# Kernel optimization log

Measured on AMD Instinct MI355X. Metric: run time of the kernel, lower is better.

Reference implementation:

```python
import jax, jax.numpy as jnp
import numpy as np

POOL = 7  # fixed 7x7 output grid, hard-coded in the original layer


def _bin_bounds(step, rlen):
    # Replicates the original bin-corner logic + empty-bin adjustment.
    i = jnp.arange(POOL, dtype=jnp.int32)
    s = i * step
    e = jnp.where(i < POOL - 1, (i + 1) * step, rlen)
    empty = s == e
    # original: grow end by 1 if room, else shrink start by 1
    e = jnp.where(empty & (e < rlen), e + 1, e)
    s = jnp.where(empty & ~(e > (i * step)) , s, s)  # no-op placeholder for clarity
    s = jnp.where(empty & ((i * step) == e), (i * step) - 1, jnp.where(empty, i * step, s))
    # simpler equivalent: if still empty after trying to grow end, shrink start
    s0 = i * step
    e0 = jnp.where(i < POOL - 1, (i + 1) * step, rlen)
    grow = empty & (e0 < rlen)
    e = jnp.where(grow, e0 + 1, e0)
    s = jnp.where(empty & ~grow, s0 - 1, s0)
    return s, e


def _pool_one(roi, fm):
    # fm: [H, W, C]; roi: [4] normalized (y1, x1, y2, x2)
    H, W, C = fm.shape
    h0 = (H * roi[0]).astype(jnp.int32)  # tf.cast to int32 truncates (floor for >=0)
    w0 = (W * roi[1]).astype(jnp.int32)
    h1 = (H * roi[2]).astype(jnp.int32)
    w1 = (W * roi[3]).astype(jnp.int32)
    rh = h1 - h0
    rw = w1 - w0
    hstep = rh // POOL
    wstep = rw // POOL
    sh, eh = _bin_bounds(hstep, rh)  # [7], region-relative
    sw, ew = _bin_bounds(wstep, rw)
    hidx = jnp.arange(H, dtype=jnp.int32)
    widx = jnp.arange(W, dtype=jnp.int32)
    rmask = (hidx[None, :] >= (h0 + sh)[:, None]) & (hidx[None, :] < (h0 + eh)[:, None])  # [7,H]
    cmask = (widx[None, :] >= (w0 + sw)[:, None]) & (widx[None, :] < (w0 + ew)[:, None])  # [7,W]
    neg = jnp.asarray(-jnp.inf, fm.dtype)
    # max over rows for each of the 7 row-bins: [7, W, C]
    t = jnp.max(jnp.where(rmask[:, :, None, None], fm[None, :, :, :], neg), axis=1)
    # max over cols for each of the 7 col-bins: [7, 7, C]
    out = jnp.max(jnp.where(cmask[None, :, :, None], t[:, None, :, :], neg), axis=2)
    return out


def setup_inputs() -> dict:
    key = jax.random.key(0)
    k_f, k_y, k_x, k_h, k_w = jax.random.split(key, 5)
    H, W, C, N = 50, 50, 1024, 300
    features = jax.random.normal(k_f, (1, H, W, C), dtype=jnp.float32)
    # well-formed normalized ROIs: y1 < y2, x1 < x2, extent in [0.2, 0.55]
    y1 = jax.random.uniform(k_y, (N,), minval=0.0, maxval=0.45)
    x1 = jax.random.uniform(k_x, (N,), minval=0.0, maxval=0.45)
    hh = jax.random.uniform(k_h, (N,), minval=0.2, maxval=0.55)
    ww = jax.random.uniform(k_w, (N,), minval=0.2, maxval=0.55)
    rois = jnp.stack([y1, x1, jnp.minimum(y1 + hh, 1.0), jnp.minimum(x1 + ww, 1.0)], axis=1).astype(jnp.float32)
    return {"features": features, "rois": rois}


def reference(features, rois):
    fm = jnp.squeeze(features, axis=0)  # [H, W, C]
    # sequential over ROIs (mirrors tf.while_loop), fully vectorized per ROI
    pooled = jax.lax.map(lambda r: _pool_one(r, fm), rois)  # [N, 7, 7, C]
    return pooled
```

## Files before the change

kernel.cpp:

```cpp
#include <hip/hip_runtime.h>
#include <math.h>

#define POOL 7
#define FH 50
#define FW 50
#define FC 1024
#define FC4 (FC / 4)
#define CHUNKS 4
#define F4C 64

typedef float vf4 __attribute__((ext_vector_type(4)));

static __device__ __forceinline__ vf4 vmax4(vf4 a, vf4 b) {
    vf4 r;
    r.x = fmaxf(a.x, b.x);
    r.y = fmaxf(a.y, b.y);
    r.z = fmaxf(a.z, b.z);
    r.w = fmaxf(a.w, b.w);
    return r;
}

__global__ __launch_bounds__(256) void roipool_kernel(
    const float* __restrict__ fm,
    const float* __restrict__ rois,
    float* __restrict__ out,
    int nbins)
{
    const int wave = threadIdx.x >> 6;
    const int lane = threadIdx.x & 63;
    const int gid  = blockIdx.x * 4 + wave;
    if (gid >= nbins) return;
    const int chunk = blockIdx.y;

    const int n  = gid / 49;
    const int ij = gid - n * 49;
    const int i  = ij / 7;
    const int j  = ij - i * 7;

    const float4 roi = reinterpret_cast<const float4*>(rois)[n];
    const int h0 = (int)((float)FH * roi.x);
    const int w0 = (int)((float)FW * roi.y);
    const int h1 = (int)((float)FH * roi.z);
    const int w1 = (int)((float)FW * roi.w);
    const int rh = h1 - h0;
    const int rw = w1 - w0;
    const int hstep = rh / POOL;
    const int wstep = rw / POOL;

    int sh = i * hstep;
    int eh = (i < POOL - 1) ? (i + 1) * hstep : rh;
    if (sh == eh) { if (eh < rh) eh += 1; else sh -= 1; }
    int sw = j * wstep;
    int ew = (j < POOL - 1) ? (j + 1) * wstep : rw;
    if (sw == ew) { if (ew < rw) ew += 1; else sw -= 1; }

    const int r0 = max(0, h0 + sh);
    const int r1 = min(FH, h0 + eh);
    const int c0 = max(0, w0 + sw);
    const int c1 = min(FW, w0 + ew);

    const int f4 = chunk * F4C + lane;

    vf4 acc = {-INFINITY, -INFINITY, -INFINITY, -INFINITY};

    const vf4* fm4 = reinterpret_cast<const vf4*>(fm);

    for (int r = r0; r < r1; ++r) {
        const vf4* rowp = fm4 + (size_t)(r * FW) * FC4 + f4;
        int c = c0;
        for (; c + 1 < c1; c += 2) {
            vf4 a = rowp[(size_t)c * FC4];
            vf4 b = rowp[(size_t)(c + 1) * FC4];
            acc = vmax4(acc, vmax4(a, b));
        }
        if (c < c1) {
            acc = vmax4(acc, rowp[(size_t)c * FC4]);
        }
    }

    vf4* o = reinterpret_cast<vf4*>(out) + (size_t)gid * FC4 + f4;
    __builtin_nontemporal_store(acc, o);
}

extern "C" void kernel_launch(void* const* d_in, const int* in_sizes, int n_in,
                              void* d_out, int out_size, void* d_ws, size_t ws_size,
                              hipStream_t stream) {
    const float* features = (const float*)d_in[0];
    const float* rois     = (const float*)d_in[1];
    float* out            = (float*)d_out;
    const int N = in_sizes[1] / 4;

    const int nbins = N * POOL * POOL;
    dim3 grid((nbins + 3) / 4, CHUNKS);
    dim3 block(256);
    roipool_kernel<<<grid, block, 0, stream>>>(features, rois, out, nbins);
}
```

Baseline: 100.8 us.

## Convert ROI pooling to persistent grid-stride loop with ROI prefetch

Replaces the one-bin-per-wave 2D grid with a fixed 2048-block persistent grid where each wave iterates over bins with a stride, prefetching the next ROI coordinates. Channel chunks are interleaved in the block index so the four chunks of a bin are launched adjacently. This aims to cut block launch overhead and improve L2 locality, but static striding may cause load imbalance since bin sizes vary.

Result: no change. 101.0 us (+0.2%).

```diff
diff --git a/kernel.cpp b/kernel.cpp
--- a/kernel.cpp
+++ b/kernel.cpp
@@ -8,6 +8,8 @@
 #define FC4 (FC / 4)
 #define CHUNKS 4
 #define F4C 64
+#define NBLOCKS 2048
+#define WSTRIDE 2048
 
 typedef float vf4 __attribute__((ext_vector_type(4)));
 
@@ -26,60 +28,72 @@
     float* __restrict__ out,
     int nbins)
 {
-    const int wave = threadIdx.x >> 6;
-    const int lane = threadIdx.x & 63;
-    const int gid  = blockIdx.x * 4 + wave;
+    const int b      = blockIdx.x;
+    const int chunk  = b & (CHUNKS - 1);
+    const int wave   = threadIdx.x >> 6;
+    const int lane   = threadIdx.x & 63;
+    const int worker = (b >> 2) * 4 + wave;
+    const int f4     = chunk * F4C + lane;
+
+    const float4* rois4 = reinterpret_cast<const float4*>(rois);
+    const vf4* fm4 = reinterpret_cast<const vf4*>(fm);
+    const size_t rowstride = (size_t)FW * FC4;
+
+    int gid = worker;
     if (gid >= nbins) return;
-    const int chunk = blockIdx.y;
 
-    const int n  = gid / 49;
-    const int ij = gid - n * 49;
-    const int i  = ij / 7;
-    const int j  = ij - i * 7;
+    float4 roi = rois4[gid / 49];
 
-    const float4 roi = reinterpret_cast<const float4*>(rois)[n];
-    const int h0 = (int)((float)FH * roi.x);
-    const int w0 = (int)((float)FW * roi.y);
-    const int h1 = (int)((float)FH * roi.z);
-    const int w1 = (int)((float)FW * roi.w);
-    const int rh = h1 - h0;
-    const int rw = w1 - w0;
-    const int hstep = rh / POOL;
-    const int wstep = rw / POOL;
+    while (gid < nbins) {
+        const int next = gid + WSTRIDE;
+        float4 roi_next;
+        if (next < nbins) roi_next = rois4[next / 49];
 
-    int sh = i * hstep;
-    int eh = (i < POOL - 1) ? (i + 1) * hstep : rh;
-    if (sh == eh) { if (eh < rh) eh += 1; else sh -= 1; }
-    int sw = j * wstep;
-    int ew = (j < POOL - 1) ? (j + 1) * wstep : rw;
-    if (sw == ew) { if (ew < rw) ew += 1; else sw -= 1; }
+        const int n  = gid / 49;
+        const int ij = gid - n * 49;
+        const int i  = ij / 7;
+        const int j  = ij - i * 7;
 
-    const int r0 = max(0, h0 + sh);
-    const int r1 = min(FH, h0 + eh);
-    const int c0 = max(0, w0 + sw);
-    const int c1 = min(FW, w0 + ew);
+        const int h0 = (int)((float)FH * roi.x);
+        const int w0 = (int)((float)FW * roi.y);
+        const int h1 = (int)((float)FH * roi.z);
+        const int w1 = (int)((float)FW * roi.w);
+        const int rh = h1 - h0;
+        const int rw = w1 - w0;
+        const int hstep = rh / POOL;
+        const int wstep = rw / POOL;
 
-    const int f4 = chunk * F4C + lane;
+        int sh = i * hstep;
+        int eh = (i < POOL - 1) ? (i + 1) * hstep : rh;
+        if (sh == eh) { if (eh < rh) eh += 1; else sh -= 1; }
+        int sw = j * wstep;
+        int ew = (j < POOL - 1) ? (j + 1) * wstep : rw;
+        if (sw == ew) { if (ew < rw) ew += 1; else sw -= 1; }
 
-    vf4 acc = {-INFINITY, -INFINITY, -INFINITY, -INFINITY};
+        const int r0 = max(0, h0 + sh);
+        const int r1 = min(FH, h0 + eh);
+        const int c0 = max(0, w0 + sw);
+        const int c1 = min(FW, w0 + ew);
 
-    const vf4* fm4 = reinterpret_cast<const vf4*>(fm);
+        vf4 acc = {-INFINITY, -INFINITY, -INFINITY, -INFINITY};
 
-    for (int r = r0; r < r1; ++r) {
-        const vf4* rowp = fm4 + (size_t)(r * FW) * FC4 + f4;
-        int c = c0;
-        for (; c + 1 < c1; c += 2) {
-            vf4 a = rowp[(size_t)c * FC4];
-            vf4 b = rowp[(size_t)(c + 1) * FC4];
-            acc = vmax4(acc, vmax4(a, b));
+        for (int r = r0; r < r1; ++r) {
+            const vf4* rp = fm4 + (size_t)r * rowstride + f4;
+            int c = c0;
+            for (; c + 1 < c1; c += 2) {
+                vf4 a0 = rp[(size_t)c * FC4];
+                vf4 a1 = rp[(size_t)(c + 1) * FC4];
+                acc = vmax4(acc, vmax4(a0, a1));
+            }
+            if (c < c1) acc = vmax4(acc, rp[(size_t)c * FC4]);
         }
-        if (c < c1) {
-            acc = vmax4(acc, rowp[(size_t)c * FC4]);
-        }
+
+        vf4* o = reinterpret_cast<vf4*>(out) + (size_t)gid * FC4 + f4;
+        __builtin_nontemporal_store(acc, o);
+
+        roi = roi_next;
+        gid = next;
     }
-
-    vf4* o = reinterpret_cast<vf4*>(out) + (size_t)gid * FC4 + f4;
-    __builtin_nontemporal_store(acc, o);
 }
 
 extern "C" void kernel_launch(void* const* d_in, const int* in_sizes, int n_in,
@@ -91,7 +105,7 @@
     const int N = in_sizes[1] / 4;
 
     const int nbins = N * POOL * POOL;
-    dim3 grid((nbins + 3) / 4, CHUNKS);
+    dim3 grid(NBLOCKS);
     dim3 block(256);
     roipool_kernel<<<grid, block, 0, stream>>>(features, rois, out, nbins);
 }
```
